# Kernel tuning notes

Hardware: AMD Instinct MI355X
Metric: run time of the kernel (lower is better)

Reference implementation:

```python
import jax, jax.numpy as jnp
import numpy as np

B, N, D, NUM_K = 128, 1024, 64, 8


def setup_inputs() -> dict:
    key = jax.random.key(0)
    k1, k2, k3 = jax.random.split(key, 3)
    nodes = jax.random.normal(k1, (B, N, D), dtype=jnp.float32)
    # xavier_uniform over (in_dims, in_dims) fan: bound = sqrt(6 / (N + N))
    bound = float(np.sqrt(6.0 / (N + N)))
    weight = jax.random.uniform(k2, (NUM_K, N, N), dtype=jnp.float32,
                                minval=-bound, maxval=bound)
    graph_shift = jax.random.normal(k3, (N, N), dtype=jnp.float32) / np.sqrt(N)
    return {"nodes": nodes, "weight": weight, "graph_shift": graph_shift}


def reference(nodes, weight, graph_shift):
    """Polynomial graph filter: out[b] = sum_k W_k @ S^k @ X_b.

    Since sum_k W_k S^k X = (sum_k W_k S^k) X, we fuse all taps into one
    N x N operator A, then apply a single batched GEMM over the batch.
    """
    n = nodes.shape[1]
    eye = jnp.eye(n, dtype=nodes.dtype)

    def step(S, Wk):
        # emit W_k @ S^k, carry S^{k+1}
        return S @ graph_shift, Wk @ S

    _, Mk = jax.lax.scan(step, eye, weight)   # [num_k, N, N]
    A = Mk.sum(axis=0)                        # fused filter operator [N, N]
    return jnp.einsum('nm,bmd->bnd', A, nodes)  # [B, N, D]
```

## Files before the change

kernel.cpp:

```cpp
#include <hip/hip_runtime.h>
#include <stdint.h>


#define NN 1024
#define NBATCH 128
#define DDIM 64

typedef float floatx4 __attribute__((ext_vector_type(4)));
typedef _Float16 f16x8 __attribute__((ext_vector_type(8)));
typedef unsigned short u16;

__device__ __forceinline__ u16 f2h(float f) {
  union { _Float16 h; u16 u; } v; v.h = (_Float16)f; return v.u;
}
__device__ __forceinline__ float h2f(u16 u) {
  union { _Float16 h; u16 u; } v; v.u = u; return (float)v.h;
}

__device__ __forceinline__ void gll16(const void* g, void* l) {
  __builtin_amdgcn_global_load_lds(
      (const __attribute__((address_space(1))) void*)g,
      (__attribute__((address_space(3))) void*)l, 16, 0, 0);
}

template <int N>
__device__ __forceinline__ void wait_vm_barrier() {
  static_assert(N == 0 || N == 4 || N == 6 || N == 8, "literal table");
  if constexpr (N == 0) asm volatile("s_waitcnt vmcnt(0)" ::: "memory");
  else if constexpr (N == 4) asm volatile("s_waitcnt vmcnt(4)" ::: "memory");
  else if constexpr (N == 6) asm volatile("s_waitcnt vmcnt(6)" ::: "memory");
  else if constexpr (N == 8) asm volatile("s_waitcnt vmcnt(8)" ::: "memory");
  asm volatile("s_barrier" ::: "memory");
}

__device__ __forceinline__ void wait_lgkm_barrier() {
  asm volatile("s_waitcnt lgkmcnt(0)" ::: "memory");
  asm volatile("s_barrier" ::: "memory");
}

template <int ROWS>
__device__ __forceinline__ void stage64(const u16* __restrict__ g, u16* lds,
                                        int wave, int lane) {
  const int r = lane >> 3, c = lane & 7;
  const int sw = (c ^ r) * 8;
#pragma unroll
  for (int i = 0; i < ROWS / 32; ++i) {
    const int rb = wave * (ROWS / 4) + i * 8;
    gll16(g + (size_t)(rb + r) * NN + sw, lds + rb * 64);
  }
}

struct CvtJob { const float* src; u16* rm; u16* cm; };
struct CvtJobs { CvtJob j[5]; };

__global__ __launch_bounds__(256) void prep_kernel(CvtJobs jobs,
                                                   const float* __restrict__ X,
                                                   u16* __restrict__ XT) {
  __shared__ u16 T[64][72];
  const int bid = blockIdx.x;
  const int t = threadIdx.x;
  if (bid < 5120) {
    CvtJob jb = jobs.j[bid >> 10];
    int idx4 = (bid & 1023) * 256 + t;
    int e = idx4 * 4;
    int row = e >> 10, col = e & (NN - 1);
    float4 f = ((const float4*)jb.src)[idx4];
    u16 h[4] = { f2h(f.x), f2h(f.y), f2h(f.z), f2h(f.w) };
    uint2 p;
    p.x = (uint32_t)h[0] | ((uint32_t)h[1] << 16);
    p.y = (uint32_t)h[2] | ((uint32_t)h[3] << 16);
    *(uint2*)&jb.rm[e] = p;
    if (jb.cm) {
#pragma unroll
      for (int i = 0; i < 4; ++i) jb.cm[(size_t)(col + i) * NN + row] = h[i];
    }
  } else {
    const int tb = bid - 5120;
    const int k0 = (tb & 15) * 64;
    const int b = tb >> 4;
#pragma unroll
    for (int it = 0; it < 4; ++it) {
      int kr = (t >> 4) + it * 16;
      int d4 = (t & 15) * 4;
      float4 f = *(const float4*)&X[((size_t)b * NN + k0 + kr) * DDIM + d4];
      T[d4 + 0][kr] = f2h(f.x);
      T[d4 + 1][kr] = f2h(f.y);
      T[d4 + 2][kr] = f2h(f.z);
      T[d4 + 3][kr] = f2h(f.w);
    }
    __syncthreads();
#pragma unroll
    for (int it = 0; it < 2; ++it) {
      int d = (t >> 3) + it * 32;
      int kc = (t & 7) * 8;
      *(uint4*)&XT[((size_t)b * DDIM + d) * NN + k0 + kc] = *(uint4*)&T[d][kc];
    }
  }
}

struct GemmJob {
  const u16* A;
  const u16* B;
  const float* addF;
  const u16* addH;
  u16* outRm;
  u16* outCm;
};
struct GemmJobs { GemmJob j[5]; };

template <int BM, int BN, int WM, int WN>
__global__ __launch_bounds__(256) void gemm_f16(GemmJobs jobs) {
  const GemmJob jb = jobs.j[blockIdx.z];
  __shared__ u16 As[2][BM * 64], Bs[2][BN * 64];
  const int t = threadIdx.x, wave = t >> 6, lane = t & 63;
  const int wm = wave / WN, wn = wave % WN;
  const int lm = lane & 15, q = lane >> 4;
  const int bm = blockIdx.x * BM, bn = blockIdx.y * BN;
  constexpr int MI = BM / (WM * 16), NI = BN / (WN * 16);
  constexpr int VMC = (BM + BN) / 32;
  floatx4 acc[MI][NI] = {};

  const u16* Ag = jb.A + (size_t)bm * NN;
  const u16* Bg = jb.B + (size_t)bn * NN;

  if (jb.addF) {
#pragma unroll
    for (int mi = 0; mi < MI; ++mi)
#pragma unroll
      for (int ni = 0; ni < NI; ++ni)
#pragma unroll
        for (int r = 0; r < 4; ++r) {
          int row = bm + wm * (BM / WM) + mi * 16 + q * 4 + r;
          int col = bn + wn * (BN / WN) + ni * 16 + lm;
          acc[mi][ni][r] = jb.addF[(size_t)row * NN + col];
        }
  } else if (jb.addH) {
#pragma unroll
    for (int mi = 0; mi < MI; ++mi)
#pragma unroll
      for (int ni = 0; ni < NI; ++ni)
#pragma unroll
        for (int r = 0; r < 4; ++r) {
          int row = bm + wm * (BM / WM) + mi * 16 + q * 4 + r;
          int col = bn + wn * (BN / WN) + ni * 16 + lm;
          acc[mi][ni][r] = h2f(jb.addH[(size_t)row * NN + col]);
        }
  }

  stage64<BM>(Ag, As[0], wave, lane);
  stage64<BN>(Bg, Bs[0], wave, lane);

  for (int kk = 0; kk < 16; ++kk) {
    const int cur = kk & 1;
    if (kk + 1 < 16) {
      stage64<BM>(Ag + (kk + 1) * 64, As[cur ^ 1], wave, lane);
      stage64<BN>(Bg + (kk + 1) * 64, Bs[cur ^ 1], wave, lane);
      wait_vm_barrier<VMC>();
    } else {
      wait_vm_barrier<0>();
    }
#pragma unroll
    for (int ks = 0; ks < 2; ++ks) {
      const int st = ((ks * 4 + q) ^ (lm & 7)) * 8;
      f16x8 bf[NI];
#pragma unroll
      for (int ni = 0; ni < NI; ++ni)
        bf[ni] = *(const f16x8*)&Bs[cur][(wn * (BN / WN) + ni * 16 + lm) * 64 + st];
#pragma unroll
      for (int mi = 0; mi < MI; ++mi) {
        f16x8 a = *(const f16x8*)&As[cur][(wm * (BM / WM) + mi * 16 + lm) * 64 + st];
#pragma unroll
        for (int ni = 0; ni < NI; ++ni)
          acc[mi][ni] = __builtin_amdgcn_mfma_f32_16x16x32_f16(a, bf[ni], acc[mi][ni], 0, 0, 0);
      }
    }
    wait_lgkm_barrier();
  }

#pragma unroll
  for (int mi = 0; mi < MI; ++mi)
#pragma unroll
    for (int ni = 0; ni < NI; ++ni)
#pragma unroll
      for (int r = 0; r < 4; ++r) {
        int row = bm + wm * (BM / WM) + mi * 16 + q * 4 + r;
        int col = bn + wn * (BN / WN) + ni * 16 + lm;
        size_t rm = (size_t)row * NN + col;
        u16 h = f2h(acc[mi][ni][r]);
        if (jb.outRm) jb.outRm[rm] = h;
        if (jb.outCm) jb.outCm[(size_t)col * NN + row] = h;
      }
}

__global__ __launch_bounds__(256) void apply_gemm(const u16* __restrict__ A,
                                                  const u16* __restrict__ XT,
                                                  float* __restrict__ out) {
  __shared__ u16 As[2][128 * 64], Xs[2][128 * 64];
  const int t = threadIdx.x, wave = t >> 6, lane = t & 63;
  const int wm = wave >> 1, wn = wave & 1;
  const int lm = lane & 15, q = lane >> 4;
  const int bn = blockIdx.x * 128;
  const int bm = blockIdx.y * 128;
  floatx4 acc[4][4] = {};
  const u16* Ag = A + (size_t)bm * NN;
  const u16* Xg = XT + (size_t)bn * NN;

  stage64<128>(Ag, As[0], wave, lane);
  stage64<128>(Xg, Xs[0], wave, lane);

  for (int kt = 0; kt < 16; ++kt) {
    const int cur = kt & 1;
    if (kt + 1 < 16) {
      stage64<128>(Ag + (kt + 1) * 64, As[cur ^ 1], wave, lane);
      stage64<128>(Xg + (kt + 1) * 64, Xs[cur ^ 1], wave, lane);
      wait_vm_barrier<8>();
    } else {
      wait_vm_barrier<0>();
    }
#pragma unroll
    for (int ks = 0; ks < 2; ++ks) {
      const int st = ((ks * 4 + q) ^ (lm & 7)) * 8;
      f16x8 xf[4];
#pragma unroll
      for (int ni = 0; ni < 4; ++ni)
        xf[ni] = *(const f16x8*)&Xs[cur][(wn * 64 + ni * 16 + lm) * 64 + st];
#pragma unroll
      for (int mi = 0; mi < 4; ++mi) {
        f16x8 a = *(const f16x8*)&As[cur][(wm * 64 + mi * 16 + lm) * 64 + st];
#pragma unroll
        for (int ni = 0; ni < 4; ++ni)
          acc[mi][ni] = __builtin_amdgcn_mfma_f32_16x16x32_f16(a, xf[ni], acc[mi][ni], 0, 0, 0);
      }
    }
    wait_lgkm_barrier();
  }

#pragma unroll
  for (int mi = 0; mi < 4; ++mi)
#pragma unroll
    for (int ni = 0; ni < 4; ++ni)
#pragma unroll
      for (int r = 0; r < 4; ++r) {
        int row = bm + wm * 64 + mi * 16 + q * 4 + r;
        int col = bn + wn * 64 + ni * 16 + lm;
        out[((size_t)(col >> 6) * NN + row) * DDIM + (col & 63)] =
            acc[mi][ni][r];
      }
}

extern "C" void kernel_launch(void* const* d_in, const int* in_sizes, int n_in,
                              void* d_out, int out_size, void* d_ws, size_t ws_size,
                              hipStream_t stream) {
  const float* nodes  = (const float*)d_in[0];
  const float* weight = (const float*)d_in[1];
  const float* gs     = (const float*)d_in[2];
  float* out = (float*)d_out;
  u16* ws = (u16*)d_ws;
  const size_t MB = (size_t)NN * NN;
  auto buf = [&](int i) -> u16* { return ws + (size_t)i * MB; };

  u16* XT = buf(16);
  CvtJobs cv{};
  cv.j[0] = { gs,              buf(0), buf(1) };
  cv.j[1] = { weight + 1 * MB, buf(2), nullptr };
  cv.j[2] = { weight + 3 * MB, buf(3), nullptr };
  cv.j[3] = { weight + 5 * MB, buf(4), nullptr };
  cv.j[4] = { weight + 7 * MB, buf(5), nullptr };
  prep_kernel<<<dim3(5120 + 2048), 256, 0, stream>>>(cv, nodes, XT);

  GemmJobs g1{};
  g1.j[0] = { buf(0), buf(1), nullptr,         nullptr, buf(6),  buf(7)  };
  g1.j[1] = { buf(2), buf(1), weight + 0 * MB, nullptr, buf(8),  nullptr };
  g1.j[2] = { buf(3), buf(1), weight + 2 * MB, nullptr, buf(9),  nullptr };
  g1.j[3] = { buf(4), buf(1), weight + 4 * MB, nullptr, buf(10), nullptr };
  g1.j[4] = { buf(5), buf(1), weight + 6 * MB, nullptr, buf(11), nullptr };
  gemm_f16<64, 128, 2, 2><<<dim3(16, 8, 5), 256, 0, stream>>>(g1);

  GemmJobs g2{};
  g2.j[0] = { buf(6),  buf(7), nullptr, nullptr, nullptr, buf(12) };
  g2.j[1] = { buf(9),  buf(7), nullptr, buf(8),  buf(13), nullptr };
  g2.j[2] = { buf(11), buf(7), nullptr, buf(10), buf(14), nullptr };
  gemm_f16<64, 64, 2, 2><<<dim3(16, 16, 3), 256, 0, stream>>>(g2);

  GemmJobs g3{};
  g3.j[0] = { buf(14), buf(12), nullptr, buf(13), buf(15), nullptr };
  gemm_f16<64, 64, 2, 2><<<dim3(16, 16, 1), 256, 0, stream>>>(g3);

  apply_gemm<<<dim3(64, 8), 256, 0, stream>>>(buf(15), XT, out);
}
```

Measured before the change: 186.9 us.

## Replace 4-wave GEMM blocks with single-wave 64x64 tiles and barrier-free prefetch

The chain GEMMs now use a single-wave 64x64 tile kernel instead of 256-thread blocks with 2x2 wave tiling. Because only one wave runs per block, the workgroup barriers go away. The kernel keeps two stages of global-to-LDS prefetch in flight, reusing the current buffer right after its fragments are read into registers. The aim is to cut synchronisation cost and overlap loads with MFMA work. In exchange, each wave does more register-heavy work, which may lower occupancy or reduce data reuse per block. Launch grids grow accordingly.

```diff
diff --git a/kernel.cpp b/kernel.cpp
--- a/kernel.cpp
+++ b/kernel.cpp
@@ -25,10 +25,8 @@
 
 template <int N>
 __device__ __forceinline__ void wait_vm_barrier() {
-  static_assert(N == 0 || N == 4 || N == 6 || N == 8, "literal table");
+  static_assert(N == 0 || N == 8, "literal table");
   if constexpr (N == 0) asm volatile("s_waitcnt vmcnt(0)" ::: "memory");
-  else if constexpr (N == 4) asm volatile("s_waitcnt vmcnt(4)" ::: "memory");
-  else if constexpr (N == 6) asm volatile("s_waitcnt vmcnt(6)" ::: "memory");
   else if constexpr (N == 8) asm volatile("s_waitcnt vmcnt(8)" ::: "memory");
   asm volatile("s_barrier" ::: "memory");
 }
@@ -108,85 +106,95 @@
 };
 struct GemmJobs { GemmJob j[5]; };
 
-template <int BM, int BN, int WM, int WN>
-__global__ __launch_bounds__(256) void gemm_f16(GemmJobs jobs) {
+__global__ __launch_bounds__(64) void gemm_sw(GemmJobs jobs) {
   const GemmJob jb = jobs.j[blockIdx.z];
-  __shared__ u16 As[2][BM * 64], Bs[2][BN * 64];
-  const int t = threadIdx.x, wave = t >> 6, lane = t & 63;
-  const int wm = wave / WN, wn = wave % WN;
+  __shared__ u16 As[2][64 * 64], Bs[2][64 * 64];
+  const int lane = threadIdx.x;
   const int lm = lane & 15, q = lane >> 4;
-  const int bm = blockIdx.x * BM, bn = blockIdx.y * BN;
-  constexpr int MI = BM / (WM * 16), NI = BN / (WN * 16);
-  constexpr int VMC = (BM + BN) / 32;
-  floatx4 acc[MI][NI] = {};
+  const int r8 = lane >> 3, c8 = lane & 7;
+  const int sw = (c8 ^ r8) * 8;
+  const int bm = blockIdx.x * 64, bn = blockIdx.y * 64;
+  floatx4 acc[4][4] = {};
 
   const u16* Ag = jb.A + (size_t)bm * NN;
   const u16* Bg = jb.B + (size_t)bn * NN;
 
   if (jb.addF) {
 #pragma unroll
-    for (int mi = 0; mi < MI; ++mi)
-#pragma unroll
-      for (int ni = 0; ni < NI; ++ni)
-#pragma unroll
-        for (int r = 0; r < 4; ++r) {
-          int row = bm + wm * (BM / WM) + mi * 16 + q * 4 + r;
-          int col = bn + wn * (BN / WN) + ni * 16 + lm;
-          acc[mi][ni][r] = jb.addF[(size_t)row * NN + col];
+    for (int mi = 0; mi < 4; ++mi)
+#pragma unroll
+      for (int ni = 0; ni < 4; ++ni)
+#pragma unroll
+        for (int rr = 0; rr < 4; ++rr) {
+          int row = bm + mi * 16 + q * 4 + rr;
+          int col = bn + ni * 16 + lm;
+          acc[mi][ni][rr] = jb.addF[(size_t)row * NN + col];
         }
   } else if (jb.addH) {
 #pragma unroll
-    for (int mi = 0; mi < MI; ++mi)
-#pragma unroll
-      for (int ni = 0; ni < NI; ++ni)
-#pragma unroll
-        for (int r = 0; r < 4; ++r) {
-          int row = bm + wm * (BM / WM) + mi * 16 + q * 4 + r;
-          int col = bn + wn * (BN / WN) + ni * 16 + lm;
-          acc[mi][ni][r] = h2f(jb.addH[(size_t)row * NN + col]);
+    for (int mi = 0; mi < 4; ++mi)
+#pragma unroll
+      for (int ni = 0; ni < 4; ++ni)
+#pragma unroll
+        for (int rr = 0; rr < 4; ++rr) {
+          int row = bm + mi * 16 + q * 4 + rr;
+          int col = bn + ni * 16 + lm;
+          acc[mi][ni][rr] = h2f(jb.addH[(size_t)row * NN + col]);
         }
   }
 
-  stage64<BM>(Ag, As[0], wave, lane);
-  stage64<BN>(Bg, Bs[0], wave, lane);
+  auto stage = [&](const u16* __restrict__ g, u16* lds) {
+#pragma unroll
+    for (int i = 0; i < 8; ++i)
+      gll16(g + (size_t)(i * 8 + r8) * NN + sw, lds + i * 8 * 64);
+  };
+
+  stage(Ag, As[0]);
+  stage(Bg, Bs[0]);
+  stage(Ag + 64, As[1]);
+  stage(Bg + 64, Bs[1]);
 
   for (int kk = 0; kk < 16; ++kk) {
     const int cur = kk & 1;
-    if (kk + 1 < 16) {
-      stage64<BM>(Ag + (kk + 1) * 64, As[cur ^ 1], wave, lane);
-      stage64<BN>(Bg + (kk + 1) * 64, Bs[cur ^ 1], wave, lane);
-      wait_vm_barrier<VMC>();
-    } else {
-      wait_vm_barrier<0>();
-    }
+    if (kk < 15)
+      asm volatile("s_waitcnt vmcnt(16)" ::: "memory");
+    else
+      asm volatile("s_waitcnt vmcnt(0)" ::: "memory");
+    f16x8 af[2][4], bf[2][4];
 #pragma unroll
     for (int ks = 0; ks < 2; ++ks) {
       const int st = ((ks * 4 + q) ^ (lm & 7)) * 8;
-      f16x8 bf[NI];
-#pragma unroll
-      for (int ni = 0; ni < NI; ++ni)
-        bf[ni] = *(const f16x8*)&Bs[cur][(wn * (BN / WN) + ni * 16 + lm) * 64 + st];
-#pragma unroll
-      for (int mi = 0; mi < MI; ++mi) {
-        f16x8 a = *(const f16x8*)&As[cur][(wm * (BM / WM) + mi * 16 + lm) * 64 + st];
-#pragma unroll
-        for (int ni = 0; ni < NI; ++ni)
-          acc[mi][ni] = __builtin_amdgcn_mfma_f32_16x16x32_f16(a, bf[ni], acc[mi][ni], 0, 0, 0);
-      }
-    }
-    wait_lgkm_barrier();
-  }
-
-#pragma unroll
-  for (int mi = 0; mi < MI; ++mi)
-#pragma unroll
-    for (int ni = 0; ni < NI; ++ni)
-#pragma unroll
-      for (int r = 0; r < 4; ++r) {
-        int row = bm + wm * (BM / WM) + mi * 16 + q * 4 + r;
-        int col = bn + wn * (BN / WN) + ni * 16 + lm;
+#pragma unroll
+      for (int i = 0; i < 4; ++i) {
+        af[ks][i] = *(const f16x8*)&As[cur][(i * 16 + lm) * 64 + st];
+        bf[ks][i] = *(const f16x8*)&Bs[cur][(i * 16 + lm) * 64 + st];
+      }
+    }
+    asm volatile("s_waitcnt lgkmcnt(0)" ::: "memory");
+    if (kk + 2 < 16) {
+      stage(Ag + (kk + 2) * 64, As[cur]);
+      stage(Bg + (kk + 2) * 64, Bs[cur]);
+    }
+#pragma unroll
+    for (int ks = 0; ks < 2; ++ks)
+#pragma unroll
+      for (int mi = 0; mi < 4; ++mi)
+#pragma unroll
+        for (int ni = 0; ni < 4; ++ni)
+          acc[mi][ni] = __builtin_amdgcn_mfma_f32_16x16x32_f16(
+              af[ks][mi], bf[ks][ni], acc[mi][ni], 0, 0, 0);
+  }
+
+#pragma unroll
+  for (int mi = 0; mi < 4; ++mi)
+#pragma unroll
+    for (int ni = 0; ni < 4; ++ni)
+#pragma unroll
+      for (int rr = 0; rr < 4; ++rr) {
+        int row = bm + mi * 16 + q * 4 + rr;
+        int col = bn + ni * 16 + lm;
         size_t rm = (size_t)row * NN + col;
-        u16 h = f2h(acc[mi][ni][r]);
+        u16 h = f2h(acc[mi][ni][rr]);
         if (jb.outRm) jb.outRm[rm] = h;
         if (jb.outCm) jb.outCm[(size_t)col * NN + row] = h;
       }
@@ -274,17 +282,17 @@
   g1.j[2] = { buf(3), buf(1), weight + 2 * MB, nullptr, buf(9),  nullptr };
   g1.j[3] = { buf(4), buf(1), weight + 4 * MB, nullptr, buf(10), nullptr };
   g1.j[4] = { buf(5), buf(1), weight + 6 * MB, nullptr, buf(11), nullptr };
-  gemm_f16<64, 128, 2, 2><<<dim3(16, 8, 5), 256, 0, stream>>>(g1);
+  gemm_sw<<<dim3(16, 16, 5), 64, 0, stream>>>(g1);
 
   GemmJobs g2{};
   g2.j[0] = { buf(6),  buf(7), nullptr, nullptr, nullptr, buf(12) };
   g2.j[1] = { buf(9),  buf(7), nullptr, buf(8),  buf(13), nullptr };
   g2.j[2] = { buf(11), buf(7), nullptr, buf(10), buf(14), nullptr };
-  gemm_f16<64, 64, 2, 2><<<dim3(16, 16, 3), 256, 0, stream>>>(g2);
+  gemm_sw<<<dim3(16, 16, 3), 64, 0, stream>>>(g2);
 
   GemmJobs g3{};
   g3.j[0] = { buf(14), buf(12), nullptr, buf(13), buf(15), nullptr };
-  gemm_f16<64, 64, 2, 2><<<dim3(16, 16, 1), 256, 0, stream>>>(g3);
+  gemm_sw<<<dim3(16, 16, 1), 64, 0, stream>>>(g3);
 
   apply_gemm<<<dim3(64, 8), 256, 0, stream>>>(buf(15), XT, out);
 }
```

Measured after the change: 199.1 us. 6.5% more time.

## Triple-buffer GEMM LDS pipeline and tile-transpose graph-shift conversion

Applied to the files above, without the earlier changes.

The generic f16 GEMM moves from a double-buffered to a triple-buffered LDS pipeline. It prefetches two K-tiles ahead, loads all fragments into registers before issuing the next global-to-LDS copy, and needs only one barrier per iteration. The prep kernel now transposes the graph-shift matrix through a shared-memory tile instead of scattered 2-byte column writes. The column-major GEMM output is written as packed 8-byte stores. The cost is more LDS per block, which may lower occupancy, and more registers held for the prefetched fragments.

```diff
diff --git a/kernel.cpp b/kernel.cpp
--- a/kernel.cpp
+++ b/kernel.cpp
@@ -24,18 +24,18 @@
 }
 
 template <int N>
-__device__ __forceinline__ void wait_vm_barrier() {
+__device__ __forceinline__ void vm_wait() {
   static_assert(N == 0 || N == 4 || N == 6 || N == 8, "literal table");
   if constexpr (N == 0) asm volatile("s_waitcnt vmcnt(0)" ::: "memory");
   else if constexpr (N == 4) asm volatile("s_waitcnt vmcnt(4)" ::: "memory");
   else if constexpr (N == 6) asm volatile("s_waitcnt vmcnt(6)" ::: "memory");
   else if constexpr (N == 8) asm volatile("s_waitcnt vmcnt(8)" ::: "memory");
+}
+__device__ __forceinline__ void barrier() {
   asm volatile("s_barrier" ::: "memory");
 }
-
-__device__ __forceinline__ void wait_lgkm_barrier() {
+__device__ __forceinline__ void lgkm0() {
   asm volatile("s_waitcnt lgkmcnt(0)" ::: "memory");
-  asm volatile("s_barrier" ::: "memory");
 }
 
 template <int ROWS>
@@ -59,23 +59,45 @@
   __shared__ u16 T[64][72];
   const int bid = blockIdx.x;
   const int t = threadIdx.x;
-  if (bid < 5120) {
-    CvtJob jb = jobs.j[bid >> 10];
-    int idx4 = (bid & 1023) * 256 + t;
+  if (bid < 256) {
+    const CvtJob jb = jobs.j[0];
+    const int tr = bid >> 4, tc = bid & 15;
+#pragma unroll
+    for (int it = 0; it < 4; ++it) {
+      int lr = (t >> 4) + it * 16;
+      int lc4 = (t & 15) * 4;
+      size_t gidx = (size_t)(tr * 64 + lr) * NN + tc * 64 + lc4;
+      float4 f = *(const float4*)&jb.src[gidx];
+      u16 h[4] = { f2h(f.x), f2h(f.y), f2h(f.z), f2h(f.w) };
+      uint2 p;
+      p.x = (uint32_t)h[0] | ((uint32_t)h[1] << 16);
+      p.y = (uint32_t)h[2] | ((uint32_t)h[3] << 16);
+      *(uint2*)&jb.rm[gidx] = p;
+      T[lc4 + 0][lr] = h[0];
+      T[lc4 + 1][lr] = h[1];
+      T[lc4 + 2][lr] = h[2];
+      T[lc4 + 3][lr] = h[3];
+    }
+    __syncthreads();
+#pragma unroll
+    for (int it = 0; it < 2; ++it) {
+      int lc = (t >> 3) + it * 32;
+      int lr8 = (t & 7) * 8;
+      *(uint4*)&jb.cm[(size_t)(tc * 64 + lc) * NN + tr * 64 + lr8] =
+          *(uint4*)&T[lc][lr8];
+    }
+  } else if (bid < 4352) {
+    const int wb = bid - 256;
+    const CvtJob jb = jobs.j[1 + (wb >> 10)];
+    int idx4 = (wb & 1023) * 256 + t;
     int e = idx4 * 4;
-    int row = e >> 10, col = e & (NN - 1);
     float4 f = ((const float4*)jb.src)[idx4];
-    u16 h[4] = { f2h(f.x), f2h(f.y), f2h(f.z), f2h(f.w) };
     uint2 p;
-    p.x = (uint32_t)h[0] | ((uint32_t)h[1] << 16);
-    p.y = (uint32_t)h[2] | ((uint32_t)h[3] << 16);
+    p.x = (uint32_t)f2h(f.x) | ((uint32_t)f2h(f.y) << 16);
+    p.y = (uint32_t)f2h(f.z) | ((uint32_t)f2h(f.w) << 16);
     *(uint2*)&jb.rm[e] = p;
-    if (jb.cm) {
-#pragma unroll
-      for (int i = 0; i < 4; ++i) jb.cm[(size_t)(col + i) * NN + row] = h[i];
-    }
   } else {
-    const int tb = bid - 5120;
+    const int tb = bid - 4352;
     const int k0 = (tb & 15) * 64;
     const int b = tb >> 4;
 #pragma unroll
@@ -111,7 +133,8 @@
 template <int BM, int BN, int WM, int WN>
 __global__ __launch_bounds__(256) void gemm_f16(GemmJobs jobs) {
   const GemmJob jb = jobs.j[blockIdx.z];
-  __shared__ u16 As[2][BM * 64], Bs[2][BN * 64];
+  __shared__ alignas(16) u16 As[3][BM * 64];
+  __shared__ alignas(16) u16 Bs[3][BN * 64];
   const int t = threadIdx.x, wave = t >> 6, lane = t & 63;
   const int wm = wave / WN, wn = wave % WN;
   const int lm = lane & 15, q = lane >> 4;
@@ -149,53 +172,65 @@
 
   stage64<BM>(Ag, As[0], wave, lane);
   stage64<BN>(Bg, Bs[0], wave, lane);
+  stage64<BM>(Ag + 64, As[1], wave, lane);
+  stage64<BN>(Bg + 64, Bs[1], wave, lane);
 
   for (int kk = 0; kk < 16; ++kk) {
-    const int cur = kk & 1;
-    if (kk + 1 < 16) {
-      stage64<BM>(Ag + (kk + 1) * 64, As[cur ^ 1], wave, lane);
-      stage64<BN>(Bg + (kk + 1) * 64, Bs[cur ^ 1], wave, lane);
-      wait_vm_barrier<VMC>();
-    } else {
-      wait_vm_barrier<0>();
-    }
+    const int cur = kk % 3;
+    if (kk < 15) vm_wait<VMC>(); else vm_wait<0>();
+    barrier();
+    f16x8 af[2][MI], bf[2][NI];
 #pragma unroll
     for (int ks = 0; ks < 2; ++ks) {
       const int st = ((ks * 4 + q) ^ (lm & 7)) * 8;
-      f16x8 bf[NI];
 #pragma unroll
       for (int ni = 0; ni < NI; ++ni)
-        bf[ni] = *(const f16x8*)&Bs[cur][(wn * (BN / WN) + ni * 16 + lm) * 64 + st];
-#pragma unroll
-      for (int mi = 0; mi < MI; ++mi) {
-        f16x8 a = *(const f16x8*)&As[cur][(wm * (BM / WM) + mi * 16 + lm) * 64 + st];
+        bf[ks][ni] = *(const f16x8*)&Bs[cur][(wn * (BN / WN) + ni * 16 + lm) * 64 + st];
+#pragma unroll
+      for (int mi = 0; mi < MI; ++mi)
+        af[ks][mi] = *(const f16x8*)&As[cur][(wm * (BM / WM) + mi * 16 + lm) * 64 + st];
+    }
+    if (kk + 2 < 16) {
+      stage64<BM>(Ag + (kk + 2) * 64, As[(kk + 2) % 3], wave, lane);
+      stage64<BN>(Bg + (kk + 2) * 64, Bs[(kk + 2) % 3], wave, lane);
+    }
+#pragma unroll
+    for (int ks = 0; ks < 2; ++ks)
+#pragma unroll
+      for (int mi = 0; mi < MI; ++mi)
 #pragma unroll
         for (int ni = 0; ni < NI; ++ni)
-          acc[mi][ni] = __builtin_amdgcn_mfma_f32_16x16x32_f16(a, bf[ni], acc[mi][ni], 0, 0, 0);
+          acc[mi][ni] = __builtin_amdgcn_mfma_f32_16x16x32_f16(
+              af[ks][mi], bf[ks][ni], acc[mi][ni], 0, 0, 0);
+  }
+
+#pragma unroll
+  for (int mi = 0; mi < MI; ++mi)
+#pragma unroll
+    for (int ni = 0; ni < NI; ++ni) {
+      int row0 = bm + wm * (BM / WM) + mi * 16 + q * 4;
+      int col = bn + wn * (BN / WN) + ni * 16 + lm;
+      u16 h[4];
+#pragma unroll
+      for (int r = 0; r < 4; ++r) h[r] = f2h(acc[mi][ni][r]);
+      if (jb.outRm) {
+#pragma unroll
+        for (int r = 0; r < 4; ++r)
+          jb.outRm[(size_t)(row0 + r) * NN + col] = h[r];
       }
-    }
-    wait_lgkm_barrier();
-  }
-
-#pragma unroll
-  for (int mi = 0; mi < MI; ++mi)
-#pragma unroll
-    for (int ni = 0; ni < NI; ++ni)
-#pragma unroll
-      for (int r = 0; r < 4; ++r) {
-        int row = bm + wm * (BM / WM) + mi * 16 + q * 4 + r;
-        int col = bn + wn * (BN / WN) + ni * 16 + lm;
-        size_t rm = (size_t)row * NN + col;
-        u16 h = f2h(acc[mi][ni][r]);
-        if (jb.outRm) jb.outRm[rm] = h;
-        if (jb.outCm) jb.outCm[(size_t)col * NN + row] = h;
+      if (jb.outCm) {
+        uint2 p;
+        p.x = (uint32_t)h[0] | ((uint32_t)h[1] << 16);
+        p.y = (uint32_t)h[2] | ((uint32_t)h[3] << 16);
+        *(uint2*)&jb.outCm[(size_t)col * NN + row0] = p;
       }
+    }
 }
 
 __global__ __launch_bounds__(256) void apply_gemm(const u16* __restrict__ A,
                                                   const u16* __restrict__ XT,
                                                   float* __restrict__ out) {
-  __shared__ u16 As[2][128 * 64], Xs[2][128 * 64];
+  __shared__ alignas(16) u16 As[2][128 * 64], Xs[2][128 * 64];
   const int t = threadIdx.x, wave = t >> 6, lane = t & 63;
   const int wm = wave >> 1, wn = wave & 1;
   const int lm = lane & 15, q = lane >> 4;
@@ -213,10 +248,11 @@
     if (kt + 1 < 16) {
       stage64<128>(Ag + (kt + 1) * 64, As[cur ^ 1], wave, lane);
       stage64<128>(Xg + (kt + 1) * 64, Xs[cur ^ 1], wave, lane);
-      wait_vm_barrier<8>();
+      vm_wait<8>();
     } else {
-      wait_vm_barrier<0>();
-    }
+      vm_wait<0>();
+    }
+    barrier();
 #pragma unroll
     for (int ks = 0; ks < 2; ++ks) {
       const int st = ((ks * 4 + q) ^ (lm & 7)) * 8;
@@ -232,7 +268,8 @@
           acc[mi][ni] = __builtin_amdgcn_mfma_f32_16x16x32_f16(a, xf[ni], acc[mi][ni], 0, 0, 0);
       }
     }
-    wait_lgkm_barrier();
+    lgkm0();
+    barrier();
   }
 
 #pragma unroll
@@ -266,7 +303,7 @@
   cv.j[2] = { weight + 3 * MB, buf(3), nullptr };
   cv.j[3] = { weight + 5 * MB, buf(4), nullptr };
   cv.j[4] = { weight + 7 * MB, buf(5), nullptr };
-  prep_kernel<<<dim3(5120 + 2048), 256, 0, stream>>>(cv, nodes, XT);
+  prep_kernel<<<dim3(6400), 256, 0, stream>>>(cv, nodes, XT);
 
   GemmJobs g1{};
   g1.j[0] = { buf(0), buf(1), nullptr,         nullptr, buf(6),  buf(7)  };
```

Result: faster. 173.2 us (-7.3%).
